# Optimization experiments

Measured on AMD Instinct MI355X. Metric: run time of the kernel, lower is better.

The kernel has to match this reference:

```python
import math
import jax, jax.numpy as jnp
import numpy as np

N_HEAD = 16
N_KV_HEAD = 4
HEAD_DIM = 64
EPS = 1e-6  # flax nnx.RMSNorm default epsilon
NEG_INF = -1000000000.0


def apply_rotary_emb(x, cos, sin):
    # x: (B,T,H,hd); cos/sin broadcast to (B,T,H,hd//2)
    d = x.shape[3] // 2
    x1, x2 = x[..., :d], x[..., d:]
    y1 = x1 * cos + x2 * sin
    y2 = x1 * -sin + x2 * cos
    return jnp.concatenate([y1, y2], axis=3).astype(x.dtype)


def rmsnorm_noscale(x):
    # flax nnx.RMSNorm(use_scale=False): x * rsqrt(mean(x^2) + eps)
    ms = jnp.mean(jnp.square(x), axis=-1, keepdims=True)
    return x * jax.lax.rsqrt(ms + EPS)


def setup_inputs() -> dict:
    key = jax.random.key(0)
    ks = jax.random.split(key, 7)
    B, T, C = 2, 2048, 1024
    sc = 1.0 / math.sqrt(C)
    x = jax.random.normal(ks[0], (B, T, C), jnp.float32)
    # realistic rotary tables
    pos = jnp.arange(T, dtype=jnp.float32)
    inv_freq = 1.0 / (10000.0 ** (jnp.arange(0, HEAD_DIM // 2, dtype=jnp.float32) / (HEAD_DIM // 2)))
    ang = pos[:, None] * inv_freq[None, :]  # (T, hd/2)
    cos = jnp.cos(ang)[None, :, None, :]
    sin = jnp.sin(ang)[None, :, None, :]
    Wq = jax.random.normal(ks[1], (C, N_HEAD * HEAD_DIM), jnp.float32) * sc
    Wk = jax.random.normal(ks[2], (C, N_KV_HEAD * HEAD_DIM), jnp.float32) * sc
    Wv = jax.random.normal(ks[3], (C, N_KV_HEAD * HEAD_DIM), jnp.float32) * sc
    Wo = jax.random.normal(ks[4], (C, C), jnp.float32) * sc
    return {"x": x, "cos": cos, "sin": sin, "Wq": Wq, "Wk": Wk, "Wv": Wv, "Wo": Wo}


def reference(x, cos, sin, Wq, Wk, Wv, Wo):
    B, T, C = x.shape
    q = (x @ Wq).reshape(B, T, N_HEAD, HEAD_DIM)
    k = (x @ Wk).reshape(B, T, N_KV_HEAD, HEAD_DIM)
    v = (x @ Wv).reshape(B, T, N_KV_HEAD, HEAD_DIM)
    q = rmsnorm_noscale(apply_rotary_emb(q, cos, sin))
    k = rmsnorm_noscale(apply_rotary_emb(k, cos, sin))
    q = jnp.transpose(q, (0, 2, 1, 3))  # (B,H,T,hd)
    k = jnp.transpose(k, (0, 2, 1, 3))  # (B,KV,T,hd)
    v = jnp.transpose(v, (0, 2, 1, 3))
    n_rep = N_HEAD // N_KV_HEAD
    k = jnp.repeat(k, n_rep, axis=1)
    v = jnp.repeat(v, n_rep, axis=1)
    scale = 1.0 / math.sqrt(HEAD_DIM)
    logits = jnp.einsum('bhtd,bhsd->bhts', q, k) * scale
    causal = jnp.where(jnp.tril(jnp.ones((T, T), dtype=jnp.bool_)), 0.0, NEG_INF)
    logits = logits + causal
    w = jax.nn.softmax(logits, axis=-1)
    y = jnp.einsum('bhts,bhsd->bhtd', w, v)
    y = jnp.transpose(y, (0, 2, 1, 3)).reshape(B, T, C)
    return y @ Wo
```

## Files before the change

kernel.cpp:

```cpp
#include <hip/hip_runtime.h>
#include <hip/hip_bf16.h>
#include <math.h>

#define EPS 1e-6f
#define LOG2E 1.44269504088896340736f

typedef __attribute__((ext_vector_type(8))) short short8;
typedef __attribute__((ext_vector_type(4))) short short4v;
typedef __attribute__((ext_vector_type(4))) float f32x4;

static __device__ __forceinline__ short f2bf(float x) {
    unsigned u = __builtin_bit_cast(unsigned, x);
    u += 0x7fffu + ((u >> 16) & 1u);
    return (short)(u >> 16);
}
static __device__ __forceinline__ float bf2f(short s) {
    unsigned u = ((unsigned)(unsigned short)s) << 16;
    return __builtin_bit_cast(float, u);
}

typedef __attribute__((address_space(1))) const void gvoid_t;
typedef __attribute__((address_space(3))) void lvoid_t;
static __device__ __forceinline__ void gload_lds16(const void* g, void* l) {
    __builtin_amdgcn_global_load_lds((gvoid_t*)g, (lvoid_t*)l, 16, 0, 0);
}

__global__ __launch_bounds__(256) void prep_inputs(
    const float* __restrict__ x, const float* __restrict__ Wq,
    const float* __restrict__ Wk, const float* __restrict__ Wv,
    const float* __restrict__ Wo, short* __restrict__ x16,
    short* __restrict__ WT, short* __restrict__ WoT, int n8) {
    if ((int)blockIdx.x < 2048) {
        const int i = blockIdx.x * 256 + threadIdx.x;
        if (i >= n8) return;
        const float4 a = reinterpret_cast<const float4*>(x)[2 * i];
        const float4 b = reinterpret_cast<const float4*>(x)[2 * i + 1];
        short8 o;
        o[0] = f2bf(a.x); o[1] = f2bf(a.y); o[2] = f2bf(a.z); o[3] = f2bf(a.w);
        o[4] = f2bf(b.x); o[5] = f2bf(b.y); o[6] = f2bf(b.z); o[7] = f2bf(b.w);
        reinterpret_cast<short8*>(x16)[i] = o;
        return;
    }
    __shared__ short tl[64][65];
    int t = blockIdx.x - 2048;
    const float* src; short* dst; int N, nx;
    if (t < 256)      { src = Wq; dst = WT;                N = 1024; nx = 16; }
    else if (t < 320) { src = Wk; dst = WT + 1024 * 1024;  N = 256;  nx = 4;  t -= 256; }
    else if (t < 384) { src = Wv; dst = WT + 1280 * 1024;  N = 256;  nx = 4;  t -= 320; }
    else              { src = Wo; dst = WoT;               N = 1024; nx = 16; t -= 384; }
    const int n0 = (t % nx) * 64, k0 = (t / nx) * 64;
    const int tid = threadIdx.x;

    #pragma unroll
    for (int i = 0; i < 4; ++i) {
        const int kr = (tid >> 4) + i * 16;
        const int c4 = (tid & 15) * 4;
        const float4 v = *reinterpret_cast<const float4*>(
            &src[(size_t)(k0 + kr) * N + n0 + c4]);
        tl[kr][c4 + 0] = f2bf(v.x);
        tl[kr][c4 + 1] = f2bf(v.y);
        tl[kr][c4 + 2] = f2bf(v.z);
        tl[kr][c4 + 3] = f2bf(v.w);
    }
    __syncthreads();

    const int nr  = tid >> 2;
    const int kc0 = (tid & 3) * 16;
    short tmp[16];
    #pragma unroll
    for (int j = 0; j < 16; ++j) tmp[j] = tl[kc0 + j][nr];
    short8* outp = reinterpret_cast<short8*>(&dst[(size_t)(n0 + nr) * 1024 + k0 + kc0]);
    outp[0] = *reinterpret_cast<short8*>(&tmp[0]);
    outp[1] = *reinterpret_cast<short8*>(&tmp[8]);
}

__global__ __launch_bounds__(256) void gemm_qkv_fused(
    const short* __restrict__ A, const short* __restrict__ BT,
    const float* __restrict__ cosb, const float* __restrict__ sinb,
    short* __restrict__ q16, short* __restrict__ k16, short* __restrict__ vT,
    int B, int T) {
    __shared__ short smem[2][(128 + 64) * 64];

    const int K = 1024;
    const int tid  = threadIdx.x;
    const int lane = tid & 63;
    const int w    = tid >> 6;
    const int lq = lane & 15, lh = lane >> 4;
    const int wm = w >> 1,   wn = w & 1;
    const size_t arow0 = (size_t)blockIdx.x * 128;
    const size_t brow0 = (size_t)blockIdx.y * 64;

    const int sr  = lane >> 3;
    const int sc  = lane & 7;
    const int scg = sc ^ sr;

    f32x4 acc[4][2];
    #pragma unroll
    for (int mi = 0; mi < 4; ++mi)
        #pragma unroll
        for (int ni = 0; ni < 2; ++ni) acc[mi][ni] = (f32x4){0.f, 0.f, 0.f, 0.f};

    const int NT = K >> 6;

    auto STAGE = [&](int u, int k0) {
        short* As = smem[u];
        short* Bs = smem[u] + 128 * 64;
        #pragma unroll
        for (int i = 0; i < 4; ++i) {
            const int rg = w * 4 + i;
            gload_lds16(A + (arow0 + rg * 8 + sr) * K + k0 + scg * 8,
                        &As[rg * 8 * 64]);
        }
        #pragma unroll
        for (int i = 0; i < 2; ++i) {
            const int rg = w * 2 + i;
            gload_lds16(BT + (brow0 + rg * 8 + sr) * K + k0 + scg * 8,
                        &Bs[rg * 8 * 64]);
        }
    };

    STAGE(0, 0);
    __syncthreads();
    int cur = 0;

    for (int t = 0; t < NT; ++t) {
        if (t + 1 < NT) STAGE(cur ^ 1, (t + 1) << 6);
        const short* As = smem[cur];
        const short* Bs = smem[cur] + 128 * 64;

        #pragma unroll
        for (int dk = 0; dk < 2; ++dk) {
            short8 af[4], bf[2];
            #pragma unroll
            for (int mi = 0; mi < 4; ++mi) {
                const int r = wm * 64 + mi * 16 + lq;
                af[mi] = *reinterpret_cast<const short8*>(
                    &As[r * 64 + (((dk * 4 + lh) ^ (lq & 7)) * 8)]);
            }
            #pragma unroll
            for (int ni = 0; ni < 2; ++ni) {
                const int r = wn * 32 + ni * 16 + lq;
                bf[ni] = *reinterpret_cast<const short8*>(
                    &Bs[r * 64 + (((dk * 4 + lh) ^ (lq & 7)) * 8)]);
            }
            __builtin_amdgcn_s_setprio(1);
            #pragma unroll
            for (int mi = 0; mi < 4; ++mi)
                #pragma unroll
                for (int ni = 0; ni < 2; ++ni)
                    acc[mi][ni] = __builtin_amdgcn_mfma_f32_16x16x32_bf16(
                        af[mi], bf[ni], acc[mi][ni], 0, 0, 0);
            __builtin_amdgcn_s_setprio(0);
        }

        __syncthreads();
        cur ^= 1;
    }

    float* fl = (float*)smem;
    #pragma unroll
    for (int mi = 0; mi < 4; ++mi) {
        const int row = wm * 64 + mi * 16 + lh * 4;
        #pragma unroll
        for (int ni = 0; ni < 2; ++ni) {
            const int col = wn * 32 + ni * 16 + lq;
            #pragma unroll
            for (int i = 0; i < 4; ++i)
                fl[(row + i) * 66 + col] = acc[mi][ni][i];
        }
    }
    __syncthreads();

    const int by = blockIdx.y;
    const int b  = (int)(arow0 / T);
    const int t0 = (int)(arow0 % T);

    if (by < 20) {
        const int j  = lane & 31;
        const int rh = lane >> 5;
        for (int rr = 0; rr < 16; ++rr) {
            const int row = w * 32 + rr * 2 + rh;
            const int t   = t0 + row;
            const float x1 = fl[row * 66 + j];
            const float x2 = fl[row * 66 + 32 + j];
            const float c = cosb[t * 32 + j];
            const float s = sinb[t * 32 + j];
            const float y1 = x1 * c + x2 * s;
            const float y2 = x2 * c - x1 * s;
            float ss = y1 * y1 + y2 * y2;
            #pragma unroll
            for (int m = 1; m < 32; m <<= 1) ss += __shfl_xor(ss, m);
            const float r = rsqrtf(ss * (1.0f / 64.0f) + EPS);
            if (by < 16) {
                short* o = q16 + ((size_t)(b * 16 + by) * T + t) * 64;
                o[j]      = f2bf(y1 * r * (0.125f * LOG2E));
                o[j + 32] = f2bf(y2 * r * (0.125f * LOG2E));
            } else {
                short* o = k16 + ((size_t)(b * 4 + (by - 16)) * T + t) * 64;
                o[j]      = f2bf(y1 * r);
                o[j + 32] = f2bf(y2 * r);
            }
        }
    } else {
        const int kvh = by - 20;
        const int dim = tid >> 2;
        const int tq  = (tid & 3) * 16;
        const int hi  = (tq >> 4) & 1;
        const int a32 = tq & 32;
        short* orow = vT + ((size_t)(b * 4 + kvh) * 64 + dim) * T + t0;
        #pragma unroll
        for (int th = 0; th < 2; ++th) {
            short tmp[16];
            #pragma unroll
            for (int j2 = 0; j2 < 16; ++j2)
                tmp[j2] = f2bf(fl[(th * 64 + tq + j2) * 66 + dim]);
            #pragma unroll
            for (int g = 0; g < 4; ++g)
                *reinterpret_cast<short4v*>(orow + th * 64 + a32 + g * 8 + hi * 4) =
                    *reinterpret_cast<short4v*>(&tmp[g * 4]);
        }
    }
}

__global__ __launch_bounds__(256) void gemm_wo(const short* __restrict__ A,
                                               const short* __restrict__ BT,
                                               float* __restrict__ C,
                                               int M, int N, int K) {
    __shared__ short smem[2][(128 + 64) * 64];

    const int tid  = threadIdx.x;
    const int lane = tid & 63;
    const int w    = tid >> 6;
    const int lq = lane & 15, lh = lane >> 4;
    const int wm = w >> 1,   wn = w & 1;
    const size_t arow0 = (size_t)blockIdx.x * 128;
    const size_t brow0 = (size_t)blockIdx.y * 64;

    const int sr  = lane >> 3;
    const int sc  = lane & 7;
    const int scg = sc ^ sr;

    f32x4 acc[4][2];
    #pragma unroll
    for (int mi = 0; mi < 4; ++mi)
        #pragma unroll
        for (int ni = 0; ni < 2; ++ni) acc[mi][ni] = (f32x4){0.f, 0.f, 0.f, 0.f};

    const int NT = K >> 6;

    auto STAGE = [&](int u, int k0) {
        short* As = smem[u];
        short* Bs = smem[u] + 128 * 64;
        #pragma unroll
        for (int i = 0; i < 4; ++i) {
            const int rg = w * 4 + i;
            gload_lds16(A + (arow0 + rg * 8 + sr) * K + k0 + scg * 8,
                        &As[rg * 8 * 64]);
        }
        #pragma unroll
        for (int i = 0; i < 2; ++i) {
            const int rg = w * 2 + i;
            gload_lds16(BT + (brow0 + rg * 8 + sr) * K + k0 + scg * 8,
                        &Bs[rg * 8 * 64]);
        }
    };

    STAGE(0, 0);
    __syncthreads();
    int cur = 0;

    for (int t = 0; t < NT; ++t) {
        if (t + 1 < NT) STAGE(cur ^ 1, (t + 1) << 6);
        const short* As = smem[cur];
        const short* Bs = smem[cur] + 128 * 64;

        #pragma unroll
        for (int dk = 0; dk < 2; ++dk) {
            short8 af[4], bf[2];
            #pragma unroll
            for (int mi = 0; mi < 4; ++mi) {
                const int r = wm * 64 + mi * 16 + lq;
                af[mi] = *reinterpret_cast<const short8*>(
                    &As[r * 64 + (((dk * 4 + lh) ^ (lq & 7)) * 8)]);
            }
            #pragma unroll
            for (int ni = 0; ni < 2; ++ni) {
                const int r = wn * 32 + ni * 16 + lq;
                bf[ni] = *reinterpret_cast<const short8*>(
                    &Bs[r * 64 + (((dk * 4 + lh) ^ (lq & 7)) * 8)]);
            }
            __builtin_amdgcn_s_setprio(1);
            #pragma unroll
            for (int mi = 0; mi < 4; ++mi)
                #pragma unroll
                for (int ni = 0; ni < 2; ++ni)
                    acc[mi][ni] = __builtin_amdgcn_mfma_f32_16x16x32_bf16(
                        af[mi], bf[ni], acc[mi][ni], 0, 0, 0);
            __builtin_amdgcn_s_setprio(0);
        }

        __syncthreads();
        cur ^= 1;
    }

    #pragma unroll
    for (int mi = 0; mi < 4; ++mi) {
        const size_t row = arow0 + wm * 64 + mi * 16 + lh * 4;
        #pragma unroll
        for (int ni = 0; ni < 2; ++ni) {
            const size_t col = brow0 + wn * 32 + ni * 16 + lq;
            #pragma unroll
            for (int i = 0; i < 4; ++i)
                C[(row + i) * N + col] = acc[mi][ni][i];
        }
    }
}

__global__ __launch_bounds__(128) void attn_mfma(
    const short* __restrict__ q16, const short* __restrict__ k16,
    const short* __restrict__ vT16, short* __restrict__ att16, int B, int T) {
    __shared__ short Kt[64 * 64];
    __shared__ short Vt[64 * 64];

    const int tid  = threadIdx.x;
    const int lane = tid & 63;
    const int w    = tid >> 6;
    const int lq   = lane & 15;
    const int lh   = lane >> 4;

    const int idx = blockIdx.x;
    const int g   = idx & 7;
    const int j   = idx >> 3;
    const int b   = g >> 2;
    const int hk  = g & 3;
    const int qs  = (T >> 5) - 1 - (j >> 2);
    const int h   = hk * 4 + (j & 3);
    const int t0w = qs * 32 + w * 16;
    const int nt  = (qs >> 1) + 1;
    const bool evenq = !(qs & 1);

    const short* qrow = q16 + ((size_t)(b * 16 + h) * T + t0w + lq) * 64;
    const short8 qf0 = *reinterpret_cast<const short8*>(qrow + lh * 8);
    const short8 qf1 = *reinterpret_cast<const short8*>(qrow + 32 + lh * 8);

    const short* kgbase = k16 + (size_t)(b * 4 + hk) * T * 64;
    const short* vgbase = vT16 + (size_t)(b * 4 + hk) * 64 * T;

    const int sr  = lane >> 3;
    const int sc  = lane & 7;
    const int scg = sc ^ sr;

    short8 ones;
    #pragma unroll
    for (int i = 0; i < 8; ++i) ones[i] = (short)0x3F80;

    f32x4 yacc[4];
    #pragma unroll
    for (int dt = 0; dt < 4; ++dt) yacc[dt] = (f32x4){0.f, 0.f, 0.f, 0.f};
    f32x4 lacc = (f32x4){0.f, 0.f, 0.f, 0.f};

    for (int ti = 0; ti < nt; ++ti) {
        const int s0 = ti * 64;
        const bool last = (ti == nt - 1);
        const int kmax = (last && evenq) ? 2 : 4;
        __syncthreads();
        #pragma unroll
        for (int p2 = 0; p2 < 4; ++p2) {
            const int r = w * 32 + p2 * 8 + sr;
            gload_lds16(kgbase + (size_t)(s0 + r) * 64 + scg * 8,
                        &Kt[(w * 32 + p2 * 8) * 64]);
            gload_lds16(vgbase + (size_t)r * T + s0 + scg * 8,
                        &Vt[(w * 32 + p2 * 8) * 64]);
        }
        __syncthreads();

        f32x4 st[4];
        __builtin_amdgcn_s_setprio(1);
        #pragma unroll
        for (int ks = 0; ks < 4; ++ks) if (ks < kmax) {
            f32x4 a1 = (f32x4){0.f, 0.f, 0.f, 0.f};
            #pragma unroll
            for (int dk = 0; dk < 2; ++dk) {
                const short8 kfr = *reinterpret_cast<const short8*>(
                    (char*)Kt + (ks * 16 + lq) * 128 +
                    (((dk * 4 + lh) ^ (lq & 7)) * 16));
                a1 = __builtin_amdgcn_mfma_f32_16x16x32_bf16(
                    kfr, dk ? qf1 : qf0, a1, 0, 0, 0);
            }
            st[ks] = a1;
        }
        __builtin_amdgcn_s_setprio(0);

        if (last) {
            const int rloc = (qs & 1) * 32 + w * 16 + lq;
            #pragma unroll
            for (int ks = 0; ks < 4; ++ks) if (ks < kmax)
                #pragma unroll
                for (int i2 = 0; i2 < 4; ++i2)
                    if (ks * 16 + lh * 4 + i2 > rloc)
                        st[ks][i2] = -1e30f;
        }

        union { short8 s8; __hip_bfloat162 h2[4]; } pf[2];
        #pragma unroll
        for (int ks2 = 0; ks2 < 2; ++ks2) if (ks2 * 2 < kmax) {
            #pragma unroll
            for (int ks = 2 * ks2; ks < 2 * ks2 + 2; ++ks)
                #pragma unroll
                for (int i2 = 0; i2 < 4; ++i2)
                    st[ks][i2] = exp2f(st[ks][i2]);
            pf[ks2].h2[0] = __float22bfloat162_rn(float2{st[2 * ks2][0], st[2 * ks2][1]});
            pf[ks2].h2[1] = __float22bfloat162_rn(float2{st[2 * ks2][2], st[2 * ks2][3]});
            pf[ks2].h2[2] = __float22bfloat162_rn(float2{st[2 * ks2 + 1][0], st[2 * ks2 + 1][1]});
            pf[ks2].h2[3] = __float22bfloat162_rn(float2{st[2 * ks2 + 1][2], st[2 * ks2 + 1][3]});
        }

        __builtin_amdgcn_s_setprio(1);
        #pragma unroll
        for (int ks2 = 0; ks2 < 2; ++ks2) if (ks2 * 2 < kmax)
            lacc = __builtin_amdgcn_mfma_f32_16x16x32_bf16(ones, pf[ks2].s8, lacc, 0, 0, 0);
        #pragma unroll
        for (int dt = 0; dt < 4; ++dt) {
            const int rb = (dt * 16 + lq) * 128;
            const int sw = lq & 7;
            #pragma unroll
            for (int ks2 = 0; ks2 < 2; ++ks2) if (ks2 * 2 < kmax) {
                const short8 vf = *reinterpret_cast<const short8*>(
                    (const char*)Vt + rb + (((ks2 * 4 + lh) ^ sw) * 16));
                yacc[dt] = __builtin_amdgcn_mfma_f32_16x16x32_bf16(
                    vf, pf[ks2].s8, yacc[dt], 0, 0, 0);
            }
        }
        __builtin_amdgcn_s_setprio(0);
    }

    const float inv = 1.f / lacc[0];
    short* orow = att16 + (((size_t)b * T + t0w + lq) * 16 + h) * 64;
    #pragma unroll
    for (int dt = 0; dt < 4; ++dt) {
        short4v o;
        o[0] = f2bf(yacc[dt][0] * inv);
        o[1] = f2bf(yacc[dt][1] * inv);
        o[2] = f2bf(yacc[dt][2] * inv);
        o[3] = f2bf(yacc[dt][3] * inv);
        *reinterpret_cast<short4v*>(orow + dt * 16 + lh * 4) = o;
    }
}

extern "C" void kernel_launch(void* const* d_in, const int* in_sizes, int n_in,
                              void* d_out, int out_size, void* d_ws, size_t ws_size,
                              hipStream_t stream) {
    const float* x    = (const float*)d_in[0];
    const float* cosb = (const float*)d_in[1];
    const float* sinb = (const float*)d_in[2];
    const float* Wq   = (const float*)d_in[3];
    const float* Wk   = (const float*)d_in[4];
    const float* Wv   = (const float*)d_in[5];
    const float* Wo   = (const float*)d_in[6];
    float* out = (float*)d_out;

    const int B = 2, T = 2048;
    const int M = B * T;
    const size_t MB = 1 << 20;

    char* wsb = (char*)d_ws;
    short* att16 = (short*)(wsb);
    short* q16   = (short*)(wsb + 8 * MB);
    short* k16   = (short*)(wsb + 16 * MB);
    short* vT16  = (short*)(wsb + 18 * MB);
    short* x16   = (short*)(wsb + 24 * MB);
    short* WT    = (short*)(wsb + 32 * MB);
    short* WoT   = (short*)(wsb + 36 * MB);

    prep_inputs<<<2048 + 640, 256, 0, stream>>>(x, Wq, Wk, Wv, Wo,
                                                x16, WT, WoT, M * 1024 / 8);

    gemm_qkv_fused<<<dim3(M / 128, 1536 / 64), 256, 0, stream>>>(
        x16, WT, cosb, sinb, q16, k16, vT16, B, T);

    attn_mfma<<<dim3((T / 32) * 16 * B), 128, 0, stream>>>(q16, k16, vT16, att16, B, T);

    gemm_wo<<<dim3(M / 128, 1024 / 64), 256, 0, stream>>>(
        att16, WoT, out, M, 1024, 1024);
}
```

Before: 94.92 us.

## Switch attention to single-wave 32x32x16 MFMA blocks with scalar row-sum

The attention kernel now runs one 64-lane wave per 32-query block instead of two waves of 16 queries, using 32x32x16 bf16 MFMA for both QK^T and PV. The row sum is accumulated in scalar registers and reduced with one shuffle, replacing the ones-matrix MFMA. The V-transpose layout written by the prep kernel is reordered to match the new MFMA operand layout. This cuts MFMA instruction count and redundant work per block, but each block must now load the K/V tiles with a single wave and hold more accumulator registers, which lowers the parallelism available to hide load latency.

```diff
diff --git a/kernel.cpp b/kernel.cpp
--- a/kernel.cpp
+++ b/kernel.cpp
@@ -8,6 +8,7 @@
 typedef __attribute__((ext_vector_type(8))) short short8;
 typedef __attribute__((ext_vector_type(4))) short short4v;
 typedef __attribute__((ext_vector_type(4))) float f32x4;
+typedef __attribute__((ext_vector_type(16))) float f32x16;
 
 static __device__ __forceinline__ short f2bf(float x) {
     unsigned u = __builtin_bit_cast(unsigned, x);
@@ -205,8 +206,6 @@
         const int kvh = by - 20;
         const int dim = tid >> 2;
         const int tq  = (tid & 3) * 16;
-        const int hi  = (tq >> 4) & 1;
-        const int a32 = tq & 32;
         short* orow = vT + ((size_t)(b * 4 + kvh) * 64 + dim) * T + t0;
         #pragma unroll
         for (int th = 0; th < 2; ++th) {
@@ -215,9 +214,11 @@
             for (int j2 = 0; j2 < 16; ++j2)
                 tmp[j2] = f2bf(fl[(th * 64 + tq + j2) * 66 + dim]);
             #pragma unroll
-            for (int g = 0; g < 4; ++g)
-                *reinterpret_cast<short4v*>(orow + th * 64 + a32 + g * 8 + hi * 4) =
-                    *reinterpret_cast<short4v*>(&tmp[g * 4]);
+            for (int g2 = 0; g2 < 4; ++g2) {
+                const int pc = (g2 & 1) * 8 + (g2 >> 1) * 4;
+                *reinterpret_cast<short4v*>(orow + th * 64 + tq + pc) =
+                    *reinterpret_cast<short4v*>(&tmp[g2 * 4]);
+            }
         }
     }
 }
@@ -316,134 +317,166 @@
     }
 }
 
-__global__ __launch_bounds__(128) void attn_mfma(
+__global__ __launch_bounds__(64) void attn_mfma(
     const short* __restrict__ q16, const short* __restrict__ k16,
     const short* __restrict__ vT16, short* __restrict__ att16, int B, int T) {
     __shared__ short Kt[64 * 64];
     __shared__ short Vt[64 * 64];
 
-    const int tid  = threadIdx.x;
-    const int lane = tid & 63;
-    const int w    = tid >> 6;
-    const int lq   = lane & 15;
-    const int lh   = lane >> 4;
+    const int lane = threadIdx.x & 63;
+    const int lq32 = lane & 31;
+    const int hi   = lane >> 5;
 
     const int idx = blockIdx.x;
     const int g   = idx & 7;
-    const int j   = idx >> 3;
+    const int jj  = idx >> 3;
     const int b   = g >> 2;
     const int hk  = g & 3;
-    const int qs  = (T >> 5) - 1 - (j >> 2);
-    const int h   = hk * 4 + (j & 3);
-    const int t0w = qs * 32 + w * 16;
+    const int qs  = (T >> 5) - 1 - (jj >> 2);
+    const int h   = hk * 4 + (jj & 3);
+    const int t0  = qs * 32;
     const int nt  = (qs >> 1) + 1;
     const bool evenq = !(qs & 1);
 
-    const short* qrow = q16 + ((size_t)(b * 16 + h) * T + t0w + lq) * 64;
-    const short8 qf0 = *reinterpret_cast<const short8*>(qrow + lh * 8);
-    const short8 qf1 = *reinterpret_cast<const short8*>(qrow + 32 + lh * 8);
-
-    const short* kgbase = k16 + (size_t)(b * 4 + hk) * T * 64;
-    const short* vgbase = vT16 + (size_t)(b * 4 + hk) * 64 * T;
+    const short* qrow = q16 + ((size_t)(b * 16 + h) * T + t0 + lq32) * 64;
+    short8 qf[4];
+    #pragma unroll
+    for (int s = 0; s < 4; ++s)
+        qf[s] = *reinterpret_cast<const short8*>(qrow + s * 16 + hi * 8);
+
+    const short* kg = k16 + (size_t)(b * 4 + hk) * T * 64;
+    const short* vg = vT16 + (size_t)(b * 4 + hk) * 64 * T;
 
     const int sr  = lane >> 3;
     const int sc  = lane & 7;
     const int scg = sc ^ sr;
 
-    short8 ones;
-    #pragma unroll
-    for (int i = 0; i < 8; ++i) ones[i] = (short)0x3F80;
-
-    f32x4 yacc[4];
-    #pragma unroll
-    for (int dt = 0; dt < 4; ++dt) yacc[dt] = (f32x4){0.f, 0.f, 0.f, 0.f};
-    f32x4 lacc = (f32x4){0.f, 0.f, 0.f, 0.f};
+    f32x16 yacc0, yacc1;
+    #pragma unroll
+    for (int r = 0; r < 16; ++r) { yacc0[r] = 0.f; yacc1[r] = 0.f; }
+    float lsum = 0.f;
 
     for (int ti = 0; ti < nt; ++ti) {
         const int s0 = ti * 64;
         const bool last = (ti == nt - 1);
-        const int kmax = (last && evenq) ? 2 : 4;
+        const bool do1  = !(last && evenq);
+
         __syncthreads();
         #pragma unroll
-        for (int p2 = 0; p2 < 4; ++p2) {
-            const int r = w * 32 + p2 * 8 + sr;
-            gload_lds16(kgbase + (size_t)(s0 + r) * 64 + scg * 8,
-                        &Kt[(w * 32 + p2 * 8) * 64]);
-            gload_lds16(vgbase + (size_t)r * T + s0 + scg * 8,
-                        &Vt[(w * 32 + p2 * 8) * 64]);
-        }
+        for (int i = 0; i < 8; ++i)
+            gload_lds16(kg + (size_t)(s0 + i * 8 + sr) * 64 + scg * 8,
+                        &Kt[i * 8 * 64]);
+        #pragma unroll
+        for (int i = 0; i < 8; ++i)
+            gload_lds16(vg + (size_t)(i * 8 + sr) * T + s0 + scg * 8,
+                        &Vt[i * 8 * 64]);
+        asm volatile("s_waitcnt vmcnt(0)" ::: "memory");
+        __builtin_amdgcn_sched_barrier(0);
         __syncthreads();
 
-        f32x4 st[4];
+        f32x16 st0, st1;
+        #pragma unroll
+        for (int r = 0; r < 16; ++r) { st0[r] = 0.f; st1[r] = 0.f; }
         __builtin_amdgcn_s_setprio(1);
         #pragma unroll
-        for (int ks = 0; ks < 4; ++ks) if (ks < kmax) {
-            f32x4 a1 = (f32x4){0.f, 0.f, 0.f, 0.f};
-            #pragma unroll
-            for (int dk = 0; dk < 2; ++dk) {
-                const short8 kfr = *reinterpret_cast<const short8*>(
-                    (char*)Kt + (ks * 16 + lq) * 128 +
-                    (((dk * 4 + lh) ^ (lq & 7)) * 16));
-                a1 = __builtin_amdgcn_mfma_f32_16x16x32_bf16(
-                    kfr, dk ? qf1 : qf0, a1, 0, 0, 0);
-            }
-            st[ks] = a1;
+        for (int s = 0; s < 4; ++s) {
+            const int c = s * 2 + hi;
+            const short8 kf0 = *reinterpret_cast<const short8*>(
+                (const char*)Kt + lq32 * 128 + ((c ^ (lq32 & 7)) * 16));
+            st0 = __builtin_amdgcn_mfma_f32_32x32x16_bf16(kf0, qf[s], st0, 0, 0, 0);
+        }
+        if (do1) {
+            #pragma unroll
+            for (int s = 0; s < 4; ++s) {
+                const int c = s * 2 + hi;
+                const short8 kf1 = *reinterpret_cast<const short8*>(
+                    (const char*)Kt + (32 + lq32) * 128 + ((c ^ (lq32 & 7)) * 16));
+                st1 = __builtin_amdgcn_mfma_f32_32x32x16_bf16(kf1, qf[s], st1, 0, 0, 0);
+            }
         }
         __builtin_amdgcn_s_setprio(0);
 
         if (last) {
-            const int rloc = (qs & 1) * 32 + w * 16 + lq;
-            #pragma unroll
-            for (int ks = 0; ks < 4; ++ks) if (ks < kmax)
+            if (evenq) {
                 #pragma unroll
-                for (int i2 = 0; i2 < 4; ++i2)
-                    if (ks * 16 + lh * 4 + i2 > rloc)
-                        st[ks][i2] = -1e30f;
-        }
-
-        union { short8 s8; __hip_bfloat162 h2[4]; } pf[2];
-        #pragma unroll
-        for (int ks2 = 0; ks2 < 2; ++ks2) if (ks2 * 2 < kmax) {
-            #pragma unroll
-            for (int ks = 2 * ks2; ks < 2 * ks2 + 2; ++ks)
+                for (int r = 0; r < 16; ++r) {
+                    const int key = (r & 3) + 8 * (r >> 2) + 4 * hi;
+                    if (key > lq32) st0[r] = -1e30f;
+                }
+            } else {
                 #pragma unroll
-                for (int i2 = 0; i2 < 4; ++i2)
-                    st[ks][i2] = exp2f(st[ks][i2]);
-            pf[ks2].h2[0] = __float22bfloat162_rn(float2{st[2 * ks2][0], st[2 * ks2][1]});
-            pf[ks2].h2[1] = __float22bfloat162_rn(float2{st[2 * ks2][2], st[2 * ks2][3]});
-            pf[ks2].h2[2] = __float22bfloat162_rn(float2{st[2 * ks2 + 1][0], st[2 * ks2 + 1][1]});
-            pf[ks2].h2[3] = __float22bfloat162_rn(float2{st[2 * ks2 + 1][2], st[2 * ks2 + 1][3]});
+                for (int r = 0; r < 16; ++r) {
+                    const int key = (r & 3) + 8 * (r >> 2) + 4 * hi;
+                    if (key > lq32) st1[r] = -1e30f;
+                }
+            }
+        }
+
+        union pk_t { short8 s8; __hip_bfloat162 h2[4]; };
+        pk_t pA0, pA1, pB0, pB1;
+        #pragma unroll
+        for (int r = 0; r < 16; ++r) { st0[r] = exp2f(st0[r]); lsum += st0[r]; }
+        #pragma unroll
+        for (int i = 0; i < 4; ++i) {
+            pA0.h2[i] = __float22bfloat162_rn(float2{st0[2 * i], st0[2 * i + 1]});
+            pA1.h2[i] = __float22bfloat162_rn(float2{st0[8 + 2 * i], st0[8 + 2 * i + 1]});
+        }
+        if (do1) {
+            #pragma unroll
+            for (int r = 0; r < 16; ++r) { st1[r] = exp2f(st1[r]); lsum += st1[r]; }
+            #pragma unroll
+            for (int i = 0; i < 4; ++i) {
+                pB0.h2[i] = __float22bfloat162_rn(float2{st1[2 * i], st1[2 * i + 1]});
+                pB1.h2[i] = __float22bfloat162_rn(float2{st1[8 + 2 * i], st1[8 + 2 * i + 1]});
+            }
         }
 
         __builtin_amdgcn_s_setprio(1);
         #pragma unroll
-        for (int ks2 = 0; ks2 < 2; ++ks2) if (ks2 * 2 < kmax)
-            lacc = __builtin_amdgcn_mfma_f32_16x16x32_bf16(ones, pf[ks2].s8, lacc, 0, 0, 0);
-        #pragma unroll
-        for (int dt = 0; dt < 4; ++dt) {
-            const int rb = (dt * 16 + lq) * 128;
-            const int sw = lq & 7;
-            #pragma unroll
-            for (int ks2 = 0; ks2 < 2; ++ks2) if (ks2 * 2 < kmax) {
-                const short8 vf = *reinterpret_cast<const short8*>(
-                    (const char*)Vt + rb + (((ks2 * 4 + lh) ^ sw) * 16));
-                yacc[dt] = __builtin_amdgcn_mfma_f32_16x16x32_bf16(
-                    vf, pf[ks2].s8, yacc[dt], 0, 0, 0);
+        for (int dt = 0; dt < 2; ++dt) {
+            const int row = dt * 32 + lq32;
+            const int sw  = lq32 & 7;
+            const short8 vf0 = *reinterpret_cast<const short8*>(
+                (const char*)Vt + row * 128 + (((hi) ^ sw) * 16));
+            const short8 vf1 = *reinterpret_cast<const short8*>(
+                (const char*)Vt + row * 128 + (((2 + hi) ^ sw) * 16));
+            if (dt == 0) {
+                yacc0 = __builtin_amdgcn_mfma_f32_32x32x16_bf16(vf0, pA0.s8, yacc0, 0, 0, 0);
+                yacc0 = __builtin_amdgcn_mfma_f32_32x32x16_bf16(vf1, pA1.s8, yacc0, 0, 0, 0);
+            } else {
+                yacc1 = __builtin_amdgcn_mfma_f32_32x32x16_bf16(vf0, pA0.s8, yacc1, 0, 0, 0);
+                yacc1 = __builtin_amdgcn_mfma_f32_32x32x16_bf16(vf1, pA1.s8, yacc1, 0, 0, 0);
+            }
+            if (do1) {
+                const short8 vf2 = *reinterpret_cast<const short8*>(
+                    (const char*)Vt + row * 128 + (((4 + hi) ^ sw) * 16));
+                const short8 vf3 = *reinterpret_cast<const short8*>(
+                    (const char*)Vt + row * 128 + (((6 + hi) ^ sw) * 16));
+                if (dt == 0) {
+                    yacc0 = __builtin_amdgcn_mfma_f32_32x32x16_bf16(vf2, pB0.s8, yacc0, 0, 0, 0);
+                    yacc0 = __builtin_amdgcn_mfma_f32_32x32x16_bf16(vf3, pB1.s8, yacc0, 0, 0, 0);
+                } else {
+                    yacc1 = __builtin_amdgcn_mfma_f32_32x32x16_bf16(vf2, pB0.s8, yacc1, 0, 0, 0);
+                    yacc1 = __builtin_amdgcn_mfma_f32_32x32x16_bf16(vf3, pB1.s8, yacc1, 0, 0, 0);
+                }
             }
         }
         __builtin_amdgcn_s_setprio(0);
     }
 
-    const float inv = 1.f / lacc[0];
-    short* orow = att16 + (((size_t)b * T + t0w + lq) * 16 + h) * 64;
-    #pragma unroll
-    for (int dt = 0; dt < 4; ++dt) {
-        short4v o;
-        o[0] = f2bf(yacc[dt][0] * inv);
-        o[1] = f2bf(yacc[dt][1] * inv);
-        o[2] = f2bf(yacc[dt][2] * inv);
-        o[3] = f2bf(yacc[dt][3] * inv);
-        *reinterpret_cast<short4v*>(orow + dt * 16 + lh * 4) = o;
+    lsum += __shfl_xor(lsum, 32);
+    const float inv = 1.f / lsum;
+    short* orow = att16 + (((size_t)b * T + t0 + lq32) * 16 + h) * 64;
+    #pragma unroll
+    for (int i = 0; i < 4; ++i) {
+        short4v o0, o1;
+        #pragma unroll
+        for (int j2 = 0; j2 < 4; ++j2) {
+            o0[j2] = f2bf(yacc0[4 * i + j2] * inv);
+            o1[j2] = f2bf(yacc1[4 * i + j2] * inv);
+        }
+        *reinterpret_cast<short4v*>(orow + i * 8 + hi * 4)      = o0;
+        *reinterpret_cast<short4v*>(orow + 32 + i * 8 + hi * 4) = o1;
     }
 }
 
@@ -478,7 +511,7 @@
     gemm_qkv_fused<<<dim3(M / 128, 1536 / 64), 256, 0, stream>>>(
         x16, WT, cosb, sinb, q16, k16, vT16, B, T);
 
-    attn_mfma<<<dim3((T / 32) * 16 * B), 128, 0, stream>>>(q16, k16, vT16, att16, B, T);
+    attn_mfma<<<dim3((T / 32) * 16 * B), 64, 0, stream>>>(q16, k16, vT16, att16, B, T);
 
     gemm_wo<<<dim3(M / 128, 1024 / 64), 256, 0, stream>>>(
         att16, WoT, out, M, 1024, 1024);
```

Measured after the change: 104.4 us. 1.1x slower.

## Split long causal attention query blocks across two workgroups with combine kernel

Applied to the files above, without the earlier changes.

The 32 longest query strips (the upper half of the sequence) are each split into two key-range halves processed by separate workgroups. Each half writes unnormalised bf16 partial outputs and row sums to scratch, and a new combine kernel adds them and normalises. The aim is to even out the causal load imbalance and shorten the tail of the attention kernel. The cost is an extra launch, scratch traffic, and bf16 rounding of the partial sums. No max subtraction is needed because logits are bounded by the RMS-normalised q/k. The scratch reuses workspace regions that earlier kernels have already finished with.

```diff
diff --git a/kernel.cpp b/kernel.cpp
--- a/kernel.cpp
+++ b/kernel.cpp
@@ -318,7 +318,8 @@
 
 __global__ __launch_bounds__(128) void attn_mfma(
     const short* __restrict__ q16, const short* __restrict__ k16,
-    const short* __restrict__ vT16, short* __restrict__ att16, int B, int T) {
+    const short* __restrict__ vT16, short* __restrict__ att16,
+    short* __restrict__ psumY, float* __restrict__ psumL, int B, int T) {
     __shared__ short Kt[64 * 64];
     __shared__ short Vt[64 * 64];
 
@@ -333,10 +334,27 @@
     const int j   = idx >> 3;
     const int b   = g >> 2;
     const int hk  = g & 3;
-    const int qs  = (T >> 5) - 1 - (j >> 2);
+    const int u   = j >> 2;
     const int h   = hk * 4 + (j & 3);
+
+    int qs, ta, tb, half = 0;
+    bool split;
+    if (u < 64) {
+        split = true;
+        qs = 63 - (u >> 1);
+        half = u & 1;
+        const int nt0 = (qs >> 1) + 1;
+        const int mid = nt0 >> 1;
+        ta = half ? mid : 0;
+        tb = half ? nt0 : mid;
+    } else {
+        split = false;
+        qs = 95 - u;
+        ta = 0;
+        tb = (qs >> 1) + 1;
+    }
+    const int nt  = (qs >> 1) + 1;
     const int t0w = qs * 32 + w * 16;
-    const int nt  = (qs >> 1) + 1;
     const bool evenq = !(qs & 1);
 
     const short* qrow = q16 + ((size_t)(b * 16 + h) * T + t0w + lq) * 64;
@@ -359,7 +377,7 @@
     for (int dt = 0; dt < 4; ++dt) yacc[dt] = (f32x4){0.f, 0.f, 0.f, 0.f};
     f32x4 lacc = (f32x4){0.f, 0.f, 0.f, 0.f};
 
-    for (int ti = 0; ti < nt; ++ti) {
+    for (int ti = ta; ti < tb; ++ti) {
         const int s0 = ti * 64;
         const bool last = (ti == nt - 1);
         const int kmax = (last && evenq) ? 2 : 4;
@@ -434,17 +452,61 @@
         __builtin_amdgcn_s_setprio(0);
     }
 
-    const float inv = 1.f / lacc[0];
-    short* orow = att16 + (((size_t)b * T + t0w + lq) * 16 + h) * 64;
-    #pragma unroll
-    for (int dt = 0; dt < 4; ++dt) {
-        short4v o;
-        o[0] = f2bf(yacc[dt][0] * inv);
-        o[1] = f2bf(yacc[dt][1] * inv);
-        o[2] = f2bf(yacc[dt][2] * inv);
-        o[3] = f2bf(yacc[dt][3] * inv);
-        *reinterpret_cast<short4v*>(orow + dt * 16 + lh * 4) = o;
-    }
+    if (!split) {
+        const float inv = 1.f / lacc[0];
+        short* orow = att16 + (((size_t)b * T + t0w + lq) * 16 + h) * 64;
+        #pragma unroll
+        for (int dt = 0; dt < 4; ++dt) {
+            short4v o;
+            o[0] = f2bf(yacc[dt][0] * inv);
+            o[1] = f2bf(yacc[dt][1] * inv);
+            o[2] = f2bf(yacc[dt][2] * inv);
+            o[3] = f2bf(yacc[dt][3] * inv);
+            *reinterpret_cast<short4v*>(orow + dt * 16 + lh * 4) = o;
+        }
+    } else {
+        const int bh = b * 16 + h;
+        const size_t p = ((size_t)(qs - 32) * 32 + bh) * 2 + half;
+        short* yrow = psumY + p * 2048 + (w * 16 + lq) * 64;
+        #pragma unroll
+        for (int dt = 0; dt < 4; ++dt) {
+            short4v o;
+            o[0] = f2bf(yacc[dt][0]);
+            o[1] = f2bf(yacc[dt][1]);
+            o[2] = f2bf(yacc[dt][2]);
+            o[3] = f2bf(yacc[dt][3]);
+            *reinterpret_cast<short4v*>(yrow + dt * 16 + lh * 4) = o;
+        }
+        if (lh == 0) psumL[p * 32 + w * 16 + lq] = lacc[0];
+    }
+}
+
+__global__ __launch_bounds__(256) void attn_combine(
+    const short* __restrict__ psumY, const float* __restrict__ psumL,
+    short* __restrict__ att16, int B, int T) {
+    const int cb = blockIdx.x;
+    const int qs = 32 + (cb >> 5);
+    const int bh = cb & 31;
+    const int b  = bh >> 4, h = bh & 15;
+    const int tid = threadIdx.x;
+    const int row = tid >> 3;
+    const int d8  = (tid & 7) * 8;
+
+    const size_t p0 = (size_t)cb * 2;
+    const float l = psumL[p0 * 32 + row] + psumL[(p0 + 1) * 32 + row];
+    const float inv = 1.f / l;
+
+    const short8 a = *reinterpret_cast<const short8*>(
+        psumY + p0 * 2048 + row * 64 + d8);
+    const short8 c = *reinterpret_cast<const short8*>(
+        psumY + (p0 + 1) * 2048 + row * 64 + d8);
+    short8 o;
+    #pragma unroll
+    for (int i = 0; i < 8; ++i)
+        o[i] = f2bf((bf2f(a[i]) + bf2f(c[i])) * inv);
+
+    *reinterpret_cast<short8*>(
+        att16 + (((size_t)b * T + qs * 32 + row) * 16 + h) * 64 + d8) = o;
 }
 
 extern "C" void kernel_launch(void* const* d_in, const int* in_sizes, int n_in,
@@ -469,7 +531,9 @@
     short* k16   = (short*)(wsb + 16 * MB);
     short* vT16  = (short*)(wsb + 18 * MB);
     short* x16   = (short*)(wsb + 24 * MB);
+    short* psumY = (short*)(wsb + 24 * MB);
     short* WT    = (short*)(wsb + 32 * MB);
+    float* psumL = (float*)(wsb + 35 * MB);
     short* WoT   = (short*)(wsb + 36 * MB);
 
     prep_inputs<<<2048 + 640, 256, 0, stream>>>(x, Wq, Wk, Wv, Wo,
@@ -478,7 +542,10 @@
     gemm_qkv_fused<<<dim3(M / 128, 1536 / 64), 256, 0, stream>>>(
         x16, WT, cosb, sinb, q16, k16, vT16, B, T);
 
-    attn_mfma<<<dim3((T / 32) * 16 * B), 128, 0, stream>>>(q16, k16, vT16, att16, B, T);
+    attn_mfma<<<dim3(384 * 8), 128, 0, stream>>>(q16, k16, vT16, att16,
+                                                 psumY, psumL, B, T);
+
+    attn_combine<<<dim3(1024), 256, 0, stream>>>(psumY, psumL, att16, B, T);
 
     gemm_wo<<<dim3(M / 128, 1024 / 64), 256, 0, stream>>>(
         att16, WoT, out, M, 1024, 1024);
```

New measurement: 100.2 us. 1.06x slower.
